# Kernel tuning notes

Hardware: AMD Instinct MI355X
Metric: run time of the kernel (lower is better)

The kernel has to match this reference:

```python
import jax, jax.numpy as jnp
import numpy as np

N_UNITS = 1024
D_K = 64
B, S = 4, 2048
NEG = 1.0e9


def setup_inputs() -> dict:
    key = jax.random.key(0)
    ks = jax.random.split(key, 11)
    k = float(np.sqrt(1.0 / N_UNITS))
    u = lambda kk, shape: jax.random.uniform(kk, shape, jnp.float32, -k, k)
    Q = jax.random.normal(ks[0], (B, S, N_UNITS), jnp.float32)
    K = jax.random.normal(ks[1], (B, S, N_UNITS), jnp.float32)
    V = jax.random.normal(ks[2], (B, S, N_UNITS), jnp.float32)
    mask = jax.random.randint(ks[3], (B, S, S), 0, 2, jnp.int32)
    return {
        "Q": Q, "K": K, "V": V, "mask": mask,
        "Wq_w": u(ks[4], (D_K, N_UNITS)), "Wq_b": u(ks[5], (D_K,)),
        "Wk_w": u(ks[6], (D_K, N_UNITS)), "Wk_b": u(ks[7], (D_K,)),
        "Wv_w": u(ks[8], (D_K, N_UNITS)), "Wv_b": u(ks[9], (D_K,)),
    }


def reference(Q, K, V, mask, Wq_w, Wq_b, Wk_w, Wk_b, Wv_w, Wv_b):
    # Linear projections (torch Linear: x @ W.T + b)
    Q_ = jnp.einsum('bsu,du->bsd', Q, Wq_w) + Wq_b  # [B,S,D_K]
    K_ = jnp.einsum('bsu,du->bsd', K, Wk_w) + Wk_b
    V_ = jnp.einsum('bsu,du->bsd', V, Wv_w) + Wv_b
    scores = jnp.einsum('bid,bjd->bij', Q_, K_) / jnp.sqrt(jnp.float32(D_K))
    m = mask.astype(jnp.float32)
    # custom multiplicative-additive mask: scores*mask - 1e9*(1-mask)
    masked = scores * m - NEG * (1.0 - m)
    attn = jax.nn.softmax(masked, axis=-1)
    # dropout p=0.0 -> identity
    return jnp.einsum('bij,bjd->bid', attn, V_)
```

## Files before the change

### kernel.cpp

```cpp
#include <hip/hip_runtime.h>
#include <stdint.h>

#define S_ 2048

typedef __bf16 bf16x8 __attribute__((ext_vector_type(8)));
typedef float f32x4 __attribute__((ext_vector_type(4)));
typedef unsigned int u32x4 __attribute__((ext_vector_type(4)));

union FragU { u32x4 u; bf16x8 v; unsigned short s[8]; };

__device__ __forceinline__ unsigned short f2bf(float f) {
    unsigned int u = __builtin_bit_cast(unsigned int, f);
    u += 0x7fffu + ((u >> 16) & 1u);
    return (unsigned short)(u >> 16);
}

__device__ __forceinline__ void gl_lds16(const void* g, void* l) {
    __builtin_amdgcn_global_load_lds(
        (const __attribute__((address_space(1))) unsigned int*)g,
        (__attribute__((address_space(3))) unsigned int*)l, 16, 0, 0);
}

__global__ __launch_bounds__(256) void cvt_w_kernel(
    const float* __restrict__ wq, const float* __restrict__ wk,
    const float* __restrict__ wv, unsigned short* __restrict__ out)
{
    int i = blockIdx.x * 256 + threadIdx.x;
    int mat = i >> 14;
    int off = (i & 16383) << 2;
    const float* src = (mat == 0) ? wq : (mat == 1) ? wk : wv;
    float4 v = *(const float4*)(src + off);
    ushort4 o;
    o.x = f2bf(v.x); o.y = f2bf(v.y); o.z = f2bf(v.z); o.w = f2bf(v.w);
    *(ushort4*)(out + mat * 65536 + off) = o;
}

__global__ __launch_bounds__(256) void mask_pack(
    const int* __restrict__ mask, unsigned long long* __restrict__ bits)
{
    int g = blockIdx.x * 256 + threadIdx.x;
    int m = mask[g];
    unsigned long long b = __ballot(m != 0);
    if ((threadIdx.x & 63) == 0) bits[g >> 6] = b;
}

__global__ __launch_bounds__(256) void proj_kernel(
    const float* __restrict__ Q, const float* __restrict__ K, const float* __restrict__ V,
    const unsigned short* __restrict__ Wb,
    const float* __restrict__ Bq, const float* __restrict__ Bk, const float* __restrict__ Bv,
    unsigned short* __restrict__ Qb, unsigned short* __restrict__ Kb,
    unsigned short* __restrict__ Vt)
{
    const int tid = threadIdx.x;
    const int w = tid >> 6, lane = tid & 63;
    const int lm = lane & 15, quad = lane >> 4;
    const int mat = blockIdx.y;
    const int row0 = blockIdx.x * 16;

    __shared__ unsigned short Xs[16 * 72];
    __shared__ unsigned short Ws[64 * 64];

    const float* X    = (mat == 0) ? Q  : (mat == 1) ? K  : V;
    const float* Bias = (mat == 0) ? Bq : (mat == 1) ? Bk : Bv;
    const unsigned short* W = Wb + mat * 65536;

    f32x4 acc = {0.f, 0.f, 0.f, 0.f};

    const int xr = tid >> 4;
    const int xc = (tid & 15) * 4;
    const float* xg = X + (row0 + xr) * 1024 + xc;
    unsigned short* xl = &Xs[xr * 72 + xc];

    const int wrr = lane >> 3;
    const int wcg = (lane & 7) ^ wrr;
    const unsigned short* wg0 = W + (w * 16 + wrr) * 1024 + wcg * 8;
    const unsigned short* wg1 = W + (w * 16 + 8 + wrr) * 1024 + wcg * 8;
    unsigned short* wl0 = &Ws[(w * 16) * 64];
    unsigned short* wl1 = &Ws[(w * 16 + 8) * 64];

    for (int s = 0; s < 16; ++s) {
        const int k0 = s * 64;
        gl_lds16(wg0 + k0, wl0);
        gl_lds16(wg1 + k0, wl1);
        float4 xv = *(const float4*)(xg + k0);
        ushort4 xb;
        xb.x = f2bf(xv.x); xb.y = f2bf(xv.y); xb.z = f2bf(xv.z); xb.w = f2bf(xv.w);
        *(ushort4*)xl = xb;
        __syncthreads();
        #pragma unroll
        for (int h = 0; h < 2; ++h) {
            FragU af, bfr;
            af.u = *(const u32x4*)&Xs[lm * 72 + h * 32 + quad * 8];
            const int cg = (quad + 4 * h) ^ (lm & 7);
            bfr.u = *(const u32x4*)&Ws[(w * 16 + lm) * 64 + cg * 8];
            acc = __builtin_amdgcn_mfma_f32_16x16x32_bf16(af.v, bfr.v, acc, 0, 0, 0);
        }
        __syncthreads();
    }

    const int col = w * 16 + lm;
    const float bias = Bias[col];
    if (mat == 2) {
        ushort4 vv;
        unsigned short* vs = (unsigned short*)&vv;
        #pragma unroll
        for (int r = 0; r < 4; ++r) vs[r] = f2bf(acc[r] + bias);
        *(ushort4*)&Vt[(row0 >> 11) * 131072 + col * 2048 + (row0 & 2047) + quad * 4] = vv;
    } else {
        unsigned short* dst = (mat == 0) ? Qb : Kb;
        #pragma unroll
        for (int r = 0; r < 4; ++r)
            dst[(row0 + quad * 4 + r) * 64 + col] = f2bf(acc[r] + bias);
    }
}

__global__ __launch_bounds__(256) void attn_kernel(
    const unsigned short* __restrict__ Qb, const unsigned short* __restrict__ Kb,
    const unsigned short* __restrict__ Vt, const unsigned long long* __restrict__ bits,
    float* __restrict__ O0out, float* __restrict__ O1part, float* __restrict__ lpart)
{
    const int tid = threadIdx.x;
    const int w = tid >> 6, lane = tid & 63;
    const int lm = lane & 15, quad = lane >> 4;
    const int q0 = blockIdx.x * 16;
    const int b = blockIdx.y;
    const int kc = blockIdx.z;

    __shared__ unsigned short Plds[4][16 * 72];
    __shared__ float Olds[4][1024];
    __shared__ float llds[4][16];

    FragU qf0, qf1;
    const unsigned short* qptr = Qb + (b * 2048 + q0 + lm) * 64 + quad * 8;
    qf0.u = *(const u32x4*)qptr;
    qf1.u = *(const u32x4*)(qptr + 32);

    f32x4 o[4];
    #pragma unroll
    for (int dt = 0; dt < 4; ++dt) { f32x4 z = {0.f,0.f,0.f,0.f}; o[dt] = z; }
    float lsum[4] = {0.f, 0.f, 0.f, 0.f};

    const int k00 = kc * 1024 + w * 256;
    const unsigned long long* bb = bits + (b * 2048 + q0) * 32;
    const unsigned short* kbase = Kb + b * 2048 * 64;
    const unsigned short* vbase = Vt + b * 131072;

    #pragma unroll
    for (int iter = 0; iter < 4; ++iter) {
        const int k0 = k00 + iter * 64;
        const int kb6 = k0 >> 6;

        f32x4 sc[4];
        #pragma unroll
        for (int ct = 0; ct < 4; ++ct) {
            const unsigned short* kptr = kbase + (k0 + ct * 16 + lm) * 64 + quad * 8;
            FragU kf0, kf1;
            kf0.u = *(const u32x4*)kptr;
            kf1.u = *(const u32x4*)(kptr + 32);
            f32x4 a = {0.f,0.f,0.f,0.f};
            a = __builtin_amdgcn_mfma_f32_16x16x32_bf16(qf0.v, kf0.v, a, 0, 0, 0);
            a = __builtin_amdgcn_mfma_f32_16x16x32_bf16(qf1.v, kf1.v, a, 0, 0, 0);
            sc[ct] = a;
        }

        unsigned long long mb[4];
        #pragma unroll
        for (int r = 0; r < 4; ++r) mb[r] = bb[(quad * 4 + r) * 32 + kb6];

        #pragma unroll
        for (int ct = 0; ct < 4; ++ct) {
            #pragma unroll
            for (int r = 0; r < 4; ++r) {
                float p = ((mb[r] >> (ct * 16 + lm)) & 1ull)
                          ? __expf(sc[ct][r] * 0.125f) : 0.f;
                sc[ct][r] = p;
                lsum[r] += p;
            }
        }

        #pragma unroll
        for (int ct = 0; ct < 4; ++ct)
            #pragma unroll
            for (int r = 0; r < 4; ++r)
                Plds[w][(quad * 4 + r) * 72 + ct * 16 + lm] = f2bf(sc[ct][r]);

        #pragma unroll
        for (int ks = 0; ks < 2; ++ks) {
            FragU pf;
            pf.u = *(const u32x4*)&Plds[w][lm * 72 + ks * 32 + quad * 8];
            #pragma unroll
            for (int dt = 0; dt < 4; ++dt) {
                FragU vf;
                vf.u = *(const u32x4*)(vbase + (dt * 16 + lm) * 2048 + k0 + ks * 32 + quad * 8);
                o[dt] = __builtin_amdgcn_mfma_f32_16x16x32_bf16(pf.v, vf.v, o[dt], 0, 0, 0);
            }
        }
    }

    #pragma unroll
    for (int r = 0; r < 4; ++r)
        #pragma unroll
        for (int off = 1; off <= 8; off <<= 1)
            lsum[r] += __shfl_xor(lsum[r], off, 64);

    #pragma unroll
    for (int dt = 0; dt < 4; ++dt)
        #pragma unroll
        for (int r = 0; r < 4; ++r)
            Olds[w][(quad * 4 + r) * 64 + dt * 16 + lm] = o[dt][r];
    if (lm == 0)
        #pragma unroll
        for (int r = 0; r < 4; ++r) llds[w][quad * 4 + r] = lsum[r];
    __syncthreads();

    float* Odst = (kc == 0) ? O0out : O1part;
    const int blk = b * 128 + blockIdx.x;
    #pragma unroll
    for (int i = 0; i < 4; ++i) {
        int e = i * 256 + tid;
        Odst[blk * 1024 + e] = Olds[0][e] + Olds[1][e] + Olds[2][e] + Olds[3][e];
    }
    if (tid < 16)
        lpart[(kc * 512 + blk) * 16 + tid] =
            llds[0][tid] + llds[1][tid] + llds[2][tid] + llds[3][tid];
}

__global__ __launch_bounds__(256) void attn_merge(
    float* __restrict__ out, const float* __restrict__ O1,
    const float* __restrict__ lpart)
{
    int idx = blockIdx.x * 256 + threadIdx.x;
    int e4 = idx * 4;
    int blk = e4 >> 10;
    int q = (e4 >> 6) & 15;
    float l = lpart[blk * 16 + q] + lpart[(512 + blk) * 16 + q];
    float inv = 1.f / l;
    float4 a = *(const float4*)&out[e4];
    float4 c = *(const float4*)&O1[e4];
    float4 r;
    r.x = (a.x + c.x) * inv; r.y = (a.y + c.y) * inv;
    r.z = (a.z + c.z) * inv; r.w = (a.w + c.w) * inv;
    *(float4*)&out[e4] = r;
}

extern "C" void kernel_launch(void* const* d_in, const int* in_sizes, int n_in,
                              void* d_out, int out_size, void* d_ws, size_t ws_size,
                              hipStream_t stream) {
    const float* Q   = (const float*)d_in[0];
    const float* K   = (const float*)d_in[1];
    const float* V   = (const float*)d_in[2];
    const int* mask  = (const int*)d_in[3];
    const float* Wq  = (const float*)d_in[4];
    const float* bq  = (const float*)d_in[5];
    const float* Wk  = (const float*)d_in[6];
    const float* bk  = (const float*)d_in[7];
    const float* Wv  = (const float*)d_in[8];
    const float* bv  = (const float*)d_in[9];
    float* out = (float*)d_out;

    char* ws = (char*)d_ws;
    unsigned short* Qb = (unsigned short*)(ws);
    unsigned short* Kb = (unsigned short*)(ws + (1u << 20));
    unsigned short* Vt = (unsigned short*)(ws + (2u << 20));
    unsigned short* Wb = (unsigned short*)(ws + (3u << 20));
    unsigned long long* bits = (unsigned long long*)(ws + 3584u * 1024);
    float* O1part = (float*)(ws + 5632u * 1024);
    float* lpart  = (float*)(ws + 7680u * 1024);

    hipLaunchKernelGGL(cvt_w_kernel, dim3(192), dim3(256), 0, stream, Wq, Wk, Wv, Wb);
    hipLaunchKernelGGL(mask_pack, dim3(65536), dim3(256), 0, stream, mask, bits);
    hipLaunchKernelGGL(proj_kernel, dim3(512, 3), dim3(256), 0, stream,
                       Q, K, V, Wb, bq, bk, bv, Qb, Kb, Vt);
    hipLaunchKernelGGL(attn_kernel, dim3(128, 4, 2), dim3(256), 0, stream,
                       Qb, Kb, Vt, bits, out, O1part, lpart);
    hipLaunchKernelGGL(attn_merge, dim3(512), dim3(256), 0, stream,
                       out, O1part, lpart);
}
```

Baseline: 252.3 us.

## Fuse mask packing, weight conversion and split-K merge into projection and attention kernels

Removes the separate weight-conversion, mask-packing and merge kernels. The projection kernel now stages a full 16x1024 bf16 X tile in LDS once and reads fp32 weights straight from global memory, converting them in registers. The attention kernel packs its own mask rows into bitmasks in LDS and uses 8 waves over the whole key range, so normalisation happens in-kernel and no split partials are written. This saves launches and the round trip of the packed mask and partials through global memory. The cost is halving the attention grid (512 blocks) and redundant fp32 weight reads per block.

```diff
diff --git a/kernel.cpp b/kernel.cpp
--- a/kernel.cpp
+++ b/kernel.cpp
@@ -15,38 +15,13 @@
     return (unsigned short)(u >> 16);
 }
 
-__device__ __forceinline__ void gl_lds16(const void* g, void* l) {
-    __builtin_amdgcn_global_load_lds(
-        (const __attribute__((address_space(1))) unsigned int*)g,
-        (__attribute__((address_space(3))) unsigned int*)l, 16, 0, 0);
-}
-
-__global__ __launch_bounds__(256) void cvt_w_kernel(
-    const float* __restrict__ wq, const float* __restrict__ wk,
-    const float* __restrict__ wv, unsigned short* __restrict__ out)
-{
-    int i = blockIdx.x * 256 + threadIdx.x;
-    int mat = i >> 14;
-    int off = (i & 16383) << 2;
-    const float* src = (mat == 0) ? wq : (mat == 1) ? wk : wv;
-    float4 v = *(const float4*)(src + off);
-    ushort4 o;
-    o.x = f2bf(v.x); o.y = f2bf(v.y); o.z = f2bf(v.z); o.w = f2bf(v.w);
-    *(ushort4*)(out + mat * 65536 + off) = o;
-}
-
-__global__ __launch_bounds__(256) void mask_pack(
-    const int* __restrict__ mask, unsigned long long* __restrict__ bits)
-{
-    int g = blockIdx.x * 256 + threadIdx.x;
-    int m = mask[g];
-    unsigned long long b = __ballot(m != 0);
-    if ((threadIdx.x & 63) == 0) bits[g >> 6] = b;
-}
-
-__global__ __launch_bounds__(256) void proj_kernel(
+__device__ __forceinline__ unsigned int pk2(float a, float b) {
+    return (unsigned int)f2bf(a) | ((unsigned int)f2bf(b) << 16);
+}
+
+__global__ __launch_bounds__(256, 4) void proj_kernel(
     const float* __restrict__ Q, const float* __restrict__ K, const float* __restrict__ V,
-    const unsigned short* __restrict__ Wb,
+    const float* __restrict__ Wq, const float* __restrict__ Wk, const float* __restrict__ Wv,
     const float* __restrict__ Bq, const float* __restrict__ Bk, const float* __restrict__ Bv,
     unsigned short* __restrict__ Qb, unsigned short* __restrict__ Kb,
     unsigned short* __restrict__ Vt)
@@ -57,48 +32,44 @@
     const int mat = blockIdx.y;
     const int row0 = blockIdx.x * 16;
 
-    __shared__ unsigned short Xs[16 * 72];
-    __shared__ unsigned short Ws[64 * 64];
+    __shared__ unsigned short Xs[16][1032];
 
     const float* X    = (mat == 0) ? Q  : (mat == 1) ? K  : V;
+    const float* W    = (mat == 0) ? Wq : (mat == 1) ? Wk : Wv;
     const float* Bias = (mat == 0) ? Bq : (mat == 1) ? Bk : Bv;
-    const unsigned short* W = Wb + mat * 65536;
-
+
+    #pragma unroll 4
+    for (int p = 0; p < 16; ++p) {
+        float4 xv = *(const float4*)(X + (row0 + p) * 1024 + tid * 4);
+        uint2 xb;
+        xb.x = pk2(xv.x, xv.y);
+        xb.y = pk2(xv.z, xv.w);
+        *(uint2*)&Xs[p][tid * 4] = xb;
+    }
+    __syncthreads();
+
+    const int col = w * 16 + lm;
+    const float* wrow = W + col * 1024;
     f32x4 acc = {0.f, 0.f, 0.f, 0.f};
 
-    const int xr = tid >> 4;
-    const int xc = (tid & 15) * 4;
-    const float* xg = X + (row0 + xr) * 1024 + xc;
-    unsigned short* xl = &Xs[xr * 72 + xc];
-
-    const int wrr = lane >> 3;
-    const int wcg = (lane & 7) ^ wrr;
-    const unsigned short* wg0 = W + (w * 16 + wrr) * 1024 + wcg * 8;
-    const unsigned short* wg1 = W + (w * 16 + 8 + wrr) * 1024 + wcg * 8;
-    unsigned short* wl0 = &Ws[(w * 16) * 64];
-    unsigned short* wl1 = &Ws[(w * 16 + 8) * 64];
-
+    #pragma unroll 4
     for (int s = 0; s < 16; ++s) {
         const int k0 = s * 64;
-        gl_lds16(wg0 + k0, wl0);
-        gl_lds16(wg1 + k0, wl1);
-        float4 xv = *(const float4*)(xg + k0);
-        ushort4 xb;
-        xb.x = f2bf(xv.x); xb.y = f2bf(xv.y); xb.z = f2bf(xv.z); xb.w = f2bf(xv.w);
-        *(ushort4*)xl = xb;
-        __syncthreads();
-        #pragma unroll
-        for (int h = 0; h < 2; ++h) {
-            FragU af, bfr;
-            af.u = *(const u32x4*)&Xs[lm * 72 + h * 32 + quad * 8];
-            const int cg = (quad + 4 * h) ^ (lm & 7);
-            bfr.u = *(const u32x4*)&Ws[(w * 16 + lm) * 64 + cg * 8];
-            acc = __builtin_amdgcn_mfma_f32_16x16x32_bf16(af.v, bfr.v, acc, 0, 0, 0);
-        }
-        __syncthreads();
-    }
-
-    const int col = w * 16 + lm;
+        FragU af0, af1, bf0, bf1;
+        af0.u = *(const u32x4*)&Xs[lm][k0 + quad * 8];
+        af1.u = *(const u32x4*)&Xs[lm][k0 + 32 + quad * 8];
+        float4 w0 = *(const float4*)(wrow + k0 + quad * 8);
+        float4 w1 = *(const float4*)(wrow + k0 + quad * 8 + 4);
+        float4 w2 = *(const float4*)(wrow + k0 + 32 + quad * 8);
+        float4 w3 = *(const float4*)(wrow + k0 + 32 + quad * 8 + 4);
+        bf0.u[0] = pk2(w0.x, w0.y); bf0.u[1] = pk2(w0.z, w0.w);
+        bf0.u[2] = pk2(w1.x, w1.y); bf0.u[3] = pk2(w1.z, w1.w);
+        bf1.u[0] = pk2(w2.x, w2.y); bf1.u[1] = pk2(w2.z, w2.w);
+        bf1.u[2] = pk2(w3.x, w3.y); bf1.u[3] = pk2(w3.z, w3.w);
+        acc = __builtin_amdgcn_mfma_f32_16x16x32_bf16(af0.v, bf0.v, acc, 0, 0, 0);
+        acc = __builtin_amdgcn_mfma_f32_16x16x32_bf16(af1.v, bf1.v, acc, 0, 0, 0);
+    }
+
     const float bias = Bias[col];
     if (mat == 2) {
         ushort4 vv;
@@ -114,21 +85,40 @@
     }
 }
 
-__global__ __launch_bounds__(256) void attn_kernel(
+__global__ __launch_bounds__(512) void attn_kernel(
     const unsigned short* __restrict__ Qb, const unsigned short* __restrict__ Kb,
-    const unsigned short* __restrict__ Vt, const unsigned long long* __restrict__ bits,
-    float* __restrict__ O0out, float* __restrict__ O1part, float* __restrict__ lpart)
+    const unsigned short* __restrict__ Vt, const int* __restrict__ mask,
+    float* __restrict__ out)
 {
     const int tid = threadIdx.x;
     const int w = tid >> 6, lane = tid & 63;
     const int lm = lane & 15, quad = lane >> 4;
     const int q0 = blockIdx.x * 16;
     const int b = blockIdx.y;
-    const int kc = blockIdx.z;
-
-    __shared__ unsigned short Plds[4][16 * 72];
-    __shared__ float Olds[4][1024];
-    __shared__ float llds[4][16];
+
+    __shared__ unsigned long long Mb[16][32];
+    __shared__ unsigned short Plds[8][16 * 72];
+    __shared__ float Olds[8][1024];
+    __shared__ float llds[8][16];
+
+    const int* mrow = mask + (b * 2048 + q0) * 2048;
+    #pragma unroll 2
+    for (int p = 0; p < 16; ++p) {
+        int m0 = mrow[p * 2048 + tid];
+        int m1 = mrow[p * 2048 + tid + 512];
+        int m2 = mrow[p * 2048 + tid + 1024];
+        int m3 = mrow[p * 2048 + tid + 1536];
+        unsigned long long b0 = __ballot(m0 != 0);
+        unsigned long long b1 = __ballot(m1 != 0);
+        unsigned long long b2 = __ballot(m2 != 0);
+        unsigned long long b3 = __ballot(m3 != 0);
+        if (lane == 0) {
+            Mb[p][w]      = b0;
+            Mb[p][w + 8]  = b1;
+            Mb[p][w + 16] = b2;
+            Mb[p][w + 24] = b3;
+        }
+    }
 
     FragU qf0, qf1;
     const unsigned short* qptr = Qb + (b * 2048 + q0 + lm) * 64 + quad * 8;
@@ -140,15 +130,15 @@
     for (int dt = 0; dt < 4; ++dt) { f32x4 z = {0.f,0.f,0.f,0.f}; o[dt] = z; }
     float lsum[4] = {0.f, 0.f, 0.f, 0.f};
 
-    const int k00 = kc * 1024 + w * 256;
-    const unsigned long long* bb = bits + (b * 2048 + q0) * 32;
     const unsigned short* kbase = Kb + b * 2048 * 64;
     const unsigned short* vbase = Vt + b * 131072;
 
+    __syncthreads();
+
     #pragma unroll
     for (int iter = 0; iter < 4; ++iter) {
-        const int k0 = k00 + iter * 64;
-        const int kb6 = k0 >> 6;
+        const int k0 = w * 256 + iter * 64;
+        const int kw = k0 >> 6;
 
         f32x4 sc[4];
         #pragma unroll
@@ -165,7 +155,7 @@
 
         unsigned long long mb[4];
         #pragma unroll
-        for (int r = 0; r < 4; ++r) mb[r] = bb[(quad * 4 + r) * 32 + kb6];
+        for (int r = 0; r < 4; ++r) mb[r] = Mb[quad * 4 + r][kw];
 
         #pragma unroll
         for (int ct = 0; ct < 4; ++ct) {
@@ -213,34 +203,18 @@
         for (int r = 0; r < 4; ++r) llds[w][quad * 4 + r] = lsum[r];
     __syncthreads();
 
-    float* Odst = (kc == 0) ? O0out : O1part;
-    const int blk = b * 128 + blockIdx.x;
-    #pragma unroll
-    for (int i = 0; i < 4; ++i) {
-        int e = i * 256 + tid;
-        Odst[blk * 1024 + e] = Olds[0][e] + Olds[1][e] + Olds[2][e] + Olds[3][e];
-    }
-    if (tid < 16)
-        lpart[(kc * 512 + blk) * 16 + tid] =
-            llds[0][tid] + llds[1][tid] + llds[2][tid] + llds[3][tid];
-}
-
-__global__ __launch_bounds__(256) void attn_merge(
-    float* __restrict__ out, const float* __restrict__ O1,
-    const float* __restrict__ lpart)
-{
-    int idx = blockIdx.x * 256 + threadIdx.x;
-    int e4 = idx * 4;
-    int blk = e4 >> 10;
-    int q = (e4 >> 6) & 15;
-    float l = lpart[blk * 16 + q] + lpart[(512 + blk) * 16 + q];
-    float inv = 1.f / l;
-    float4 a = *(const float4*)&out[e4];
-    float4 c = *(const float4*)&O1[e4];
-    float4 r;
-    r.x = (a.x + c.x) * inv; r.y = (a.y + c.y) * inv;
-    r.z = (a.z + c.z) * inv; r.w = (a.w + c.w) * inv;
-    *(float4*)&out[e4] = r;
+    #pragma unroll
+    for (int i = 0; i < 2; ++i) {
+        int e = i * 512 + tid;
+        int q = e >> 6, d = e & 63;
+        float L = 0.f, val = 0.f;
+        #pragma unroll
+        for (int ww = 0; ww < 8; ++ww) {
+            L   += llds[ww][q];
+            val += Olds[ww][q * 64 + d];
+        }
+        out[(b * 2048 + q0 + q) * 64 + d] = val / L;
+    }
 }
 
 extern "C" void kernel_launch(void* const* d_in, const int* in_sizes, int n_in,
@@ -262,17 +236,9 @@
     unsigned short* Qb = (unsigned short*)(ws);
     unsigned short* Kb = (unsigned short*)(ws + (1u << 20));
     unsigned short* Vt = (unsigned short*)(ws + (2u << 20));
-    unsigned short* Wb = (unsigned short*)(ws + (3u << 20));
-    unsigned long long* bits = (unsigned long long*)(ws + 3584u * 1024);
-    float* O1part = (float*)(ws + 5632u * 1024);
-    float* lpart  = (float*)(ws + 7680u * 1024);
-
-    hipLaunchKernelGGL(cvt_w_kernel, dim3(192), dim3(256), 0, stream, Wq, Wk, Wv, Wb);
-    hipLaunchKernelGGL(mask_pack, dim3(65536), dim3(256), 0, stream, mask, bits);
+
     hipLaunchKernelGGL(proj_kernel, dim3(512, 3), dim3(256), 0, stream,
-                       Q, K, V, Wb, bq, bk, bv, Qb, Kb, Vt);
-    hipLaunchKernelGGL(attn_kernel, dim3(128, 4, 2), dim3(256), 0, stream,
-                       Qb, Kb, Vt, bits, out, O1part, lpart);
-    hipLaunchKernelGGL(attn_merge, dim3(512), dim3(256), 0, stream,
-                       out, O1part, lpart);
-}
+                       Q, K, V, Wq, Wk, Wv, bq, bk, bv, Qb, Kb, Vt);
+    hipLaunchKernelGGL(attn_kernel, dim3(128, 4), dim3(512), 0, stream,
+                       Qb, Kb, Vt, mask, out);
+}
```

Result: no change. 254.3 us (+0.8%).
